# Optimization experiments

Measured on AMD Instinct MI355X. Metric: run time of the kernel, lower is better.

## Reference

```python
import jax, jax.numpy as jnp
import numpy as np

B, S, D_MODEL, H = 2, 2048, 1024, 16
HD = D_MODEL // H  # 64


def rotate_half(x):
    # pairs (x_even, x_odd) -> (-x_odd, x_even), interleaved back
    x1 = x[..., ::2]
    x2 = x[..., 1::2]
    return jnp.stack([-x2, x1], axis=-1).reshape(x.shape)


def rope_sin_cos(seq_len, head_dim):
    pos = jnp.arange(seq_len, dtype=jnp.float32)
    dim = jnp.arange(head_dim, dtype=jnp.float32)
    theta = 10000.0 ** (-2.0 * jnp.floor(dim / 2.0) / head_dim)
    angles = pos[:, None] * theta[None, :]  # [S, HD]
    return jnp.sin(angles), jnp.cos(angles)


def setup_inputs():
    key = jax.random.key(0)
    ks = jax.random.split(key, 6)
    w_scale = 1.0 / np.sqrt(D_MODEL)
    x = jax.random.normal(ks[0], (B, S, D_MODEL), jnp.float32)
    # causal mask: 1.0 where attention is disallowed (j > i)
    mask = (1.0 - jnp.tril(jnp.ones((S, S), jnp.float32)))[None, None, :, :]
    wq = jax.random.normal(ks[1], (D_MODEL, D_MODEL), jnp.float32) * w_scale
    wk = jax.random.normal(ks[2], (D_MODEL, D_MODEL), jnp.float32) * w_scale
    wv = jax.random.normal(ks[3], (D_MODEL, D_MODEL), jnp.float32) * w_scale
    wo = jax.random.normal(ks[4], (D_MODEL, D_MODEL), jnp.float32) * w_scale
    zeros = jnp.zeros((D_MODEL,), jnp.float32)
    return dict(x=x, mask=mask, wq=wq, bq=zeros, wk=wk, bk=zeros,
                wv=wv, bv=zeros, wo=wo, bo=zeros)


def reference(x, mask, wq, bq, wk, bk, wv, bv, wo, bo):
    b, s, _ = x.shape

    def split_heads(t):  # [B,S,D] -> [B,H,S,HD]
        return t.reshape(b, s, H, HD).transpose(0, 2, 1, 3)

    q = split_heads(x @ wq + bq)
    k = split_heads(x @ wk + bk)
    v = split_heads(x @ wv + bv)

    sin, cos = rope_sin_cos(s, HD)
    sin = sin[None, None, :, :]
    cos = cos[None, None, :, :]
    q = q * cos + rotate_half(q) * sin
    k = k * cos + rotate_half(k) * sin

    logits = jnp.einsum('bhqd,bhkd->bhqk', q, k) / jnp.sqrt(jnp.float32(HD))
    logits = logits + mask * (-1e9)
    attn = jax.nn.softmax(logits, axis=-1)
    out = jnp.einsum('bhqk,bhkd->bhqd', attn, v)  # [B,H,S,HD]
    out = out.transpose(0, 2, 1, 3).reshape(b, s, D_MODEL)
    return out @ wo + bo
```

## Files before the change

kernel.cpp:

```cpp
#include <hip/hip_runtime.h>
#include <hip/hip_bf16.h>


#define S_ 2048
#define DM 1024
#define HD 64

typedef __attribute__((ext_vector_type(8))) short short8;
typedef __attribute__((ext_vector_type(4))) short short4v;
typedef __attribute__((ext_vector_type(4))) float floatx4;

__device__ __forceinline__ unsigned short f2b(float x) {
  union { __hip_bfloat16 h; unsigned short u; } cv;
  cv.h = __float2bfloat16(x);
  return cv.u;
}

__device__ __forceinline__ void gload_lds16(const unsigned short* g, unsigned short* l) {
  typedef const __attribute__((address_space(1))) unsigned int* gp_t;
  typedef __attribute__((address_space(3))) unsigned int* lp_t;
  __builtin_amdgcn_global_load_lds((gp_t)(const void*)g, (lp_t)(void*)l, 16, 0, 0);
}

__global__ void cast_kernel(const float* __restrict__ in,
                            unsigned short* __restrict__ out, int n) {
  int i = (blockIdx.x * blockDim.x + threadIdx.x) * 4;
  if (i >= n) return;
  float4 v = *(const float4*)(in + i);
  ushort4 o;
  o.x = f2b(v.x); o.y = f2b(v.y); o.z = f2b(v.z); o.w = f2b(v.w);
  *(ushort4*)(out + i) = o;
}

__global__ void trans_kernel(const float* __restrict__ w0, const float* __restrict__ w1,
                             const float* __restrict__ w2, const float* __restrict__ w3,
                             unsigned short* __restrict__ wt) {
  __shared__ float tile[32][33];
  const float* W = (blockIdx.z == 0) ? w0 : (blockIdx.z == 1) ? w1
                   : (blockIdx.z == 2) ? w2 : w3;
  unsigned short* Wt = wt + (size_t)blockIdx.z * DM * DM;
  const int tx = threadIdx.x & 31;
  const int ty = threadIdx.x >> 5;
  const int k0 = blockIdx.x * 32;
  const int c0 = blockIdx.y * 32;
#pragma unroll
  for (int i = 0; i < 4; ++i)
    tile[ty + i * 8][tx] = W[(size_t)(k0 + ty + i * 8) * DM + c0 + tx];
  __syncthreads();
#pragma unroll
  for (int i = 0; i < 4; ++i)
    Wt[(size_t)(c0 + ty + i * 8) * DM + k0 + tx] = f2b(tile[tx][ty + i * 8]);
}

__global__ void rope_kernel(float2* __restrict__ tab) {
  int i = blockIdx.x * 256 + threadIdx.x;
  int s = i >> 5, d2 = i & 31;
  float th = expf(-(float)d2 * (9.210340371976184f / 32.0f));
  float sn, cs;
  sincosf((float)s * th, &sn, &cs);
  tab[i] = make_float2(cs, sn);
}

__global__ __launch_bounds__(256, 3) void gemm_qkv(
    const unsigned short* __restrict__ A, const unsigned short* __restrict__ Wt,
    const float* __restrict__ bq, const float* __restrict__ bk,
    const float* __restrict__ bv, const float2* __restrict__ rope,
    unsigned short* __restrict__ QKV) {
  __shared__ __attribute__((aligned(16))) unsigned short As[128 * 64];
  __shared__ __attribute__((aligned(16))) unsigned short Bs[128 * 64];
  const int r0 = blockIdx.x * 128;
  const int c0 = blockIdx.y * 128;
  const int t = threadIdx.x;
  const int lane = t & 63;
  const int wv = t >> 6;
  const int wr = (wv >> 1) * 64;
  const int wc = (wv & 1) * 64;
  const int lr = lane & 15;
  const int lg = lane >> 4;

  const int srow = wv * 32 + (lane >> 3);
  const int sseg = ((lane & 7) ^ (lane >> 3)) * 8;
  const unsigned short* Ag = A + (size_t)(r0 + srow) * DM + sseg;
  const unsigned short* Bg = Wt + (size_t)(c0 + srow) * DM + sseg;
  unsigned short* lA = &As[wv * 32 * 64];
  unsigned short* lB = &Bs[wv * 32 * 64];

  floatx4 acc[4][4] = {};
  const int fswz = (lr & 7) << 4;

  for (int k0 = 0; k0 < DM; k0 += 64) {
#pragma unroll
    for (int j = 0; j < 4; ++j) {
      gload_lds16(Ag + k0 + j * 8 * DM, lA + j * 8 * 64);
      gload_lds16(Bg + k0 + j * 8 * DM, lB + j * 8 * 64);
    }
    __syncthreads();
#pragma unroll
    for (int kk = 0; kk < 2; ++kk) {
      short8 af[4], bf[4];
#pragma unroll
      for (int m = 0; m < 4; ++m)
        af[m] = *(const short8*)((char*)As + (wr + m * 16 + lr) * 128 +
                                 ((kk * 64 + lg * 16) ^ fswz));
#pragma unroll
      for (int n = 0; n < 4; ++n)
        bf[n] = *(const short8*)((char*)Bs + (wc + n * 16 + lr) * 128 +
                                 ((kk * 64 + lg * 16) ^ fswz));
#pragma unroll
      for (int m = 0; m < 4; ++m)
#pragma unroll
        for (int n = 0; n < 4; ++n)
          acc[m][n] = __builtin_amdgcn_mfma_f32_16x16x32_bf16(af[m], bf[n], acc[m][n], 0, 0, 0);
    }
    __syncthreads();
  }

  const int mat = blockIdx.y >> 3;
  const float* bias = (mat == 0) ? bq : (mat == 1) ? bk : bv;
  const int rbase = r0 + wr + lg * 4;
  const int cbase = c0 + wc + lr;
#pragma unroll
  for (int n = 0; n < 4; ++n) {
    const int c = cbase + n * 16;
    const int cc = c & (DM - 1);
    const float bvv = bias[cc];
    const int d = c & 63;
    const int h = cc >> 6;
#pragma unroll
    for (int m = 0; m < 4; ++m) {
#pragma unroll
      for (int i = 0; i < 4; ++i) {
        const int r = rbase + m * 16 + i;
        const int s = r & (S_ - 1);
        const int b = r >> 11;
        float v = acc[m][n][i] + bvv;
        float pv = __shfl_xor(v, 1);
        if (mat < 2) {
          float2 cssn = rope[s * 32 + (d >> 1)];
          v = (d & 1) ? fmaf(v, cssn.x, pv * cssn.y) : fmaf(v, cssn.x, -pv * cssn.y);
          if (mat == 0) v *= 0.18033688011112042f;
        }
        QKV[((size_t)((mat << 5) | (b << 4) | h) * S_ + s) * HD + d] = f2b(v);
      }
    }
  }
}

__global__ __launch_bounds__(256, 3) void gemm_out(
    const unsigned short* __restrict__ A, const unsigned short* __restrict__ Wt,
    const float* __restrict__ bias, float* __restrict__ out) {
  __shared__ __attribute__((aligned(16))) unsigned short As[128 * 64];
  __shared__ __attribute__((aligned(16))) unsigned short Bs[128 * 64];
  const int r0 = blockIdx.x * 128;
  const int c0 = blockIdx.y * 128;
  const int t = threadIdx.x;
  const int lane = t & 63;
  const int wv = t >> 6;
  const int wr = (wv >> 1) * 64;
  const int wc = (wv & 1) * 64;
  const int lr = lane & 15;
  const int lg = lane >> 4;

  const int srow = wv * 32 + (lane >> 3);
  const int sseg = ((lane & 7) ^ (lane >> 3)) * 8;
  const unsigned short* Ag = A + (size_t)(r0 + srow) * DM + sseg;
  const unsigned short* Bg = Wt + (size_t)(c0 + srow) * DM + sseg;
  unsigned short* lA = &As[wv * 32 * 64];
  unsigned short* lB = &Bs[wv * 32 * 64];

  floatx4 acc[4][4] = {};
  const int fswz = (lr & 7) << 4;

  for (int k0 = 0; k0 < DM; k0 += 64) {
#pragma unroll
    for (int j = 0; j < 4; ++j) {
      gload_lds16(Ag + k0 + j * 8 * DM, lA + j * 8 * 64);
      gload_lds16(Bg + k0 + j * 8 * DM, lB + j * 8 * 64);
    }
    __syncthreads();
#pragma unroll
    for (int kk = 0; kk < 2; ++kk) {
      short8 af[4], bf[4];
#pragma unroll
      for (int m = 0; m < 4; ++m)
        af[m] = *(const short8*)((char*)As + (wr + m * 16 + lr) * 128 +
                                 ((kk * 64 + lg * 16) ^ fswz));
#pragma unroll
      for (int n = 0; n < 4; ++n)
        bf[n] = *(const short8*)((char*)Bs + (wc + n * 16 + lr) * 128 +
                                 ((kk * 64 + lg * 16) ^ fswz));
#pragma unroll
      for (int m = 0; m < 4; ++m)
#pragma unroll
        for (int n = 0; n < 4; ++n)
          acc[m][n] = __builtin_amdgcn_mfma_f32_16x16x32_bf16(af[m], bf[n], acc[m][n], 0, 0, 0);
    }
    __syncthreads();
  }

  const int rbase = r0 + wr + lg * 4;
  const int cbase = c0 + wc + lr;
#pragma unroll
  for (int n = 0; n < 4; ++n) {
    const int c = cbase + n * 16;
    const float bvv = bias[c];
#pragma unroll
    for (int m = 0; m < 4; ++m) {
#pragma unroll
      for (int i = 0; i < 4; ++i) {
        const int r = rbase + m * 16 + i;
        out[(size_t)r * DM + c] = acc[m][n][i] + bvv;
      }
    }
  }
}

__global__ __launch_bounds__(512, 4) void attn_kernel(
    const unsigned short* __restrict__ Q, const unsigned short* __restrict__ K,
    const unsigned short* __restrict__ V, unsigned short* __restrict__ AttnC) {
  __shared__ __attribute__((aligned(16))) unsigned short Ks[2][64 * 64];
  __shared__ __attribute__((aligned(16))) unsigned short Vs[2][64 * 64];
  __shared__ __attribute__((aligned(16))) unsigned short Ps[8][16 * 64];

  const int bh = blockIdx.x;
  const int qt = 15 - (int)blockIdx.y;
  const int tid = threadIdx.x;
  const int w = tid >> 6;
  const int l = tid & 63;
  const int lg = l >> 4;
  const int lr = l & 15;
  const size_t base = (size_t)bh * S_ * HD;
  const int NT = 2 * qt + 2;
  const int dt = 2 * qt + (w >> 2);
  const int qin = ((w & 3) << 4) + lr;

  short8 qf[2];
  {
    const unsigned short* Qrow =
        Q + base + (size_t)(qt * 128 + w * 16 + lr) * HD + lg * 8;
    qf[0] = *(const short8*)(Qrow);
    qf[1] = *(const short8*)(Qrow + 32);
  }

  floatx4 o[4] = {};
  float m = -1e30f, lsum = 0.f;

  const int krow = tid >> 3;
  const int kseg = tid & 7;
  const int kp = tid & 31;
  const int vd0 = ((tid >> 5) & 7) * 8 + (tid >> 8) * 4;

  int4 kr;
  short4v va, vb;
  {
    const unsigned short* Kg = K + base;
    const unsigned short* Vg = V + base;
    kr = *(const int4*)(Kg + krow * 64 + kseg * 8);
    va = *(const short4v*)(Vg + 2 * kp * 64 + vd0);
    vb = *(const short4v*)(Vg + (2 * kp + 1) * 64 + vd0);
  }

  char* const Pw = (char*)Ps[w];
  const int pswz = (lr & 7) << 4;

  for (int t = 0; t < NT; ++t) {
    const int cur = t & 1;
    {
      char* Kb = (char*)Ks[cur];
      *(int4*)(Kb + krow * 128 + ((kseg * 16) ^ ((krow & 7) << 4))) = kr;
      char* Vb = (char*)Vs[cur];
#pragma unroll
      for (int jj = 0; jj < 4; ++jj) {
        int d = vd0 + jj;
        unsigned int pk = (unsigned int)(unsigned short)va[jj] |
                          ((unsigned int)(unsigned short)vb[jj] << 16);
        *(unsigned int*)(Vb + d * 128 + ((4 * kp) ^ ((d & 7) << 4))) = pk;
      }
    }
    if (t + 1 < NT) {
      const unsigned short* Kg = K + base + (size_t)(t + 1) * 64 * HD;
      const unsigned short* Vg = V + base + (size_t)(t + 1) * 64 * HD;
      kr = *(const int4*)(Kg + krow * 64 + kseg * 8);
      va = *(const short4v*)(Vg + 2 * kp * 64 + vd0);
      vb = *(const short4v*)(Vg + (2 * kp + 1) * 64 + vd0);
    }
    __syncthreads();
    if (t > dt) continue;

    floatx4 s[4] = {};
    __builtin_amdgcn_s_setprio(1);
#pragma unroll
    for (int kk = 0; kk < 2; ++kk) {
#pragma unroll
      for (int n = 0; n < 4; ++n) {
        int r = n * 16 + lr;
        short8 kf = *(const short8*)((char*)Ks[cur] + r * 128 +
                                     ((kk * 64 + lg * 16) ^ ((r & 7) << 4)));
        s[n] = __builtin_amdgcn_mfma_f32_16x16x32_bf16(kf, qf[kk], s[n], 0, 0, 0);
      }
    }
    __builtin_amdgcn_s_setprio(0);
    if (t == dt) {
#pragma unroll
      for (int n = 0; n < 4; ++n)
#pragma unroll
        for (int i = 0; i < 4; ++i)
          if (n * 16 + lg * 4 + i > qin) s[n][i] = -1e30f;
    }

    float tm0 = fmaxf(fmaxf(s[0][0], s[0][1]), fmaxf(s[0][2], s[0][3]));
    float tm1 = fmaxf(fmaxf(s[1][0], s[1][1]), fmaxf(s[1][2], s[1][3]));
    float tm2 = fmaxf(fmaxf(s[2][0], s[2][1]), fmaxf(s[2][2], s[2][3]));
    float tm3 = fmaxf(fmaxf(s[3][0], s[3][1]), fmaxf(s[3][2], s[3][3]));
    float tm = fmaxf(fmaxf(tm0, tm1), fmaxf(tm2, tm3));
    tm = fmaxf(tm, __shfl_xor(tm, 16));
    tm = fmaxf(tm, __shfl_xor(tm, 32));
    if (__any(tm > m + 8.f)) {
      const float mn = fmaxf(m, tm);
      const float al = exp2f(m - mn);
      m = mn;
      lsum *= al;
#pragma unroll
      for (int dd = 0; dd < 4; ++dd) o[dd] *= al;
    }
    float ps = 0.f;
#pragma unroll
    for (int n = 0; n < 4; ++n) {
#pragma unroll
      for (int i = 0; i < 4; ++i) {
        float p = exp2f(s[n][i] - m);
        s[n][i] = p;
        ps += p;
      }
    }
    lsum += ps;

#pragma unroll
    for (int n = 0; n < 4; ++n) {
#pragma unroll
      for (int h = 0; h < 2; ++h) {
        unsigned int pk = (unsigned int)f2b(s[n][2 * h]) |
                          ((unsigned int)f2b(s[n][2 * h + 1]) << 16);
        *(unsigned int*)(Pw + lr * 128 + (((n * 16 + lg * 4 + 2 * h) * 2) ^ pswz)) = pk;
      }
    }
    short8 pb[2];
#pragma unroll
    for (int kk = 0; kk < 2; ++kk)
      pb[kk] = *(const short8*)(Pw + lr * 128 + ((kk * 64 + lg * 16) ^ pswz));
    __builtin_amdgcn_s_setprio(1);
#pragma unroll
    for (int kk = 0; kk < 2; ++kk)
#pragma unroll
      for (int dd = 0; dd < 4; ++dd) {
        int d = dd * 16 + lr;
        short8 vbf = *(const short8*)((char*)Vs[cur] + d * 128 +
                                      ((kk * 64 + lg * 16) ^ ((d & 7) << 4)));
        o[dd] = __builtin_amdgcn_mfma_f32_16x16x32_bf16(vbf, pb[kk], o[dd], 0, 0, 0);
      }
    __builtin_amdgcn_s_setprio(0);
  }

  lsum += __shfl_xor(lsum, 16);
  lsum += __shfl_xor(lsum, 32);
  const float inv = 1.f / lsum;
  unsigned short* orow =
      AttnC + (size_t)((bh >> 4) * S_ + qt * 128 + w * 16 + lr) * DM + (bh & 15) * HD;
#pragma unroll
  for (int dd = 0; dd < 4; ++dd) {
    unsigned int w0 = (unsigned int)f2b(o[dd][0] * inv) |
                      ((unsigned int)f2b(o[dd][1] * inv) << 16);
    unsigned int w1 = (unsigned int)f2b(o[dd][2] * inv) |
                      ((unsigned int)f2b(o[dd][3] * inv) << 16);
    *(uint2*)(orow + dd * 16 + lg * 4) = make_uint2(w0, w1);
  }
}

extern "C" void kernel_launch(void* const* d_in, const int* in_sizes, int n_in,
                              void* d_out, int out_size, void* d_ws, size_t ws_size,
                              hipStream_t stream) {
  const float* x = (const float*)d_in[0];
  const float* wq = (const float*)d_in[2];
  const float* bq = (const float*)d_in[3];
  const float* wk = (const float*)d_in[4];
  const float* bk = (const float*)d_in[5];
  const float* wv = (const float*)d_in[6];
  const float* bv = (const float*)d_in[7];
  const float* wo = (const float*)d_in[8];
  const float* bo = (const float*)d_in[9];

  char* ws = (char*)d_ws;
  const size_t MB = 1024ull * 1024ull;
  unsigned short* Xc = (unsigned short*)(ws);
  unsigned short* Wt = (unsigned short*)(ws + 8 * MB);
  unsigned short* QKVb = (unsigned short*)(ws + 16 * MB);
  unsigned short* Ac = (unsigned short*)(ws + 40 * MB);
  float2* rope = (float2*)(ws + 48 * MB);

  cast_kernel<<<4096, 256, 0, stream>>>(x, Xc, 2 * S_ * DM);
  trans_kernel<<<dim3(32, 32, 4), 256, 0, stream>>>(wq, wk, wv, wo, Wt);
  rope_kernel<<<256, 256, 0, stream>>>(rope);
  gemm_qkv<<<dim3(32, 24), 256, 0, stream>>>(Xc, Wt, bq, bk, bv, rope, QKVb);
  attn_kernel<<<dim3(32, 16), 512, 0, stream>>>(
      QKVb, QKVb + 32ull * S_ * HD, QKVb + 64ull * S_ * HD, Ac);
  gemm_out<<<dim3(32, 8), 256, 0, stream>>>(Ac, Wt + 3ull * DM * DM, bo, (float*)d_out);
}
```

Baseline: 120.5 us.

## Merge prep kernels into one launch and load K fragments directly from global

The cast, weight-transpose and RoPE-table kernels are combined into one prep kernel that dispatches on block index, removing two kernel launches and their gaps. Separately, the attention kernel stops staging K tiles through LDS. Each wave now loads its K MFMA fragments straight from global memory (L2) right before use, which frees LDS space and drops the LDS stores and swizzled reads. In exchange, K loads are no longer prefetched a tile ahead, and the eight waves of a block each read the same K tile redundantly, which may expose global-load latency in the inner loop.

```diff
diff --git a/kernel.cpp b/kernel.cpp
--- a/kernel.cpp
+++ b/kernel.cpp
@@ -22,43 +22,46 @@
   __builtin_amdgcn_global_load_lds((gp_t)(const void*)g, (lp_t)(void*)l, 16, 0, 0);
 }
 
-__global__ void cast_kernel(const float* __restrict__ in,
-                            unsigned short* __restrict__ out, int n) {
-  int i = (blockIdx.x * blockDim.x + threadIdx.x) * 4;
-  if (i >= n) return;
-  float4 v = *(const float4*)(in + i);
-  ushort4 o;
-  o.x = f2b(v.x); o.y = f2b(v.y); o.z = f2b(v.z); o.w = f2b(v.w);
-  *(ushort4*)(out + i) = o;
-}
-
-__global__ void trans_kernel(const float* __restrict__ w0, const float* __restrict__ w1,
-                             const float* __restrict__ w2, const float* __restrict__ w3,
-                             unsigned short* __restrict__ wt) {
-  __shared__ float tile[32][33];
-  const float* W = (blockIdx.z == 0) ? w0 : (blockIdx.z == 1) ? w1
-                   : (blockIdx.z == 2) ? w2 : w3;
-  unsigned short* Wt = wt + (size_t)blockIdx.z * DM * DM;
-  const int tx = threadIdx.x & 31;
-  const int ty = threadIdx.x >> 5;
-  const int k0 = blockIdx.x * 32;
-  const int c0 = blockIdx.y * 32;
-#pragma unroll
-  for (int i = 0; i < 4; ++i)
-    tile[ty + i * 8][tx] = W[(size_t)(k0 + ty + i * 8) * DM + c0 + tx];
-  __syncthreads();
-#pragma unroll
-  for (int i = 0; i < 4; ++i)
-    Wt[(size_t)(c0 + ty + i * 8) * DM + k0 + tx] = f2b(tile[tx][ty + i * 8]);
-}
-
-__global__ void rope_kernel(float2* __restrict__ tab) {
-  int i = blockIdx.x * 256 + threadIdx.x;
-  int s = i >> 5, d2 = i & 31;
-  float th = expf(-(float)d2 * (9.210340371976184f / 32.0f));
-  float sn, cs;
-  sincosf((float)s * th, &sn, &cs);
-  tab[i] = make_float2(cs, sn);
+__global__ void prep_kernel(const float* __restrict__ x,
+                            const float* __restrict__ w0, const float* __restrict__ w1,
+                            const float* __restrict__ w2, const float* __restrict__ w3,
+                            unsigned short* __restrict__ xc,
+                            unsigned short* __restrict__ wt,
+                            float2* __restrict__ rope) {
+  const int bid = blockIdx.x;
+  if (bid < 4096) {
+    int i = (bid * 256 + threadIdx.x) * 4;
+    float4 v = *(const float4*)(x + i);
+    ushort4 o;
+    o.x = f2b(v.x); o.y = f2b(v.y); o.z = f2b(v.z); o.w = f2b(v.w);
+    *(ushort4*)(xc + i) = o;
+  } else if (bid < 8192) {
+    __shared__ float tile[32][33];
+    const int rem = bid - 4096;
+    const int z = rem >> 10;
+    const int bx = (rem & 1023) & 31;
+    const int by = (rem & 1023) >> 5;
+    const float* W = (z == 0) ? w0 : (z == 1) ? w1 : (z == 2) ? w2 : w3;
+    unsigned short* Wt = wt + (size_t)z * DM * DM;
+    const int tx = threadIdx.x & 31;
+    const int ty = threadIdx.x >> 5;
+    const int k0 = bx * 32;
+    const int c0 = by * 32;
+#pragma unroll
+    for (int i = 0; i < 4; ++i)
+      tile[ty + i * 8][tx] = W[(size_t)(k0 + ty + i * 8) * DM + c0 + tx];
+    __syncthreads();
+#pragma unroll
+    for (int i = 0; i < 4; ++i)
+      Wt[(size_t)(c0 + ty + i * 8) * DM + k0 + tx] = f2b(tile[tx][ty + i * 8]);
+  } else {
+    int i = (bid - 8192) * 256 + threadIdx.x;
+    int s = i >> 5, d2 = i & 31;
+    float th = expf(-(float)d2 * (9.210340371976184f / 32.0f));
+    float sn, cs;
+    sincosf((float)s * th, &sn, &cs);
+    rope[i] = make_float2(cs, sn);
+  }
 }
 
 __global__ __launch_bounds__(256, 3) void gemm_qkv(
@@ -218,7 +221,6 @@
 __global__ __launch_bounds__(512, 4) void attn_kernel(
     const unsigned short* __restrict__ Q, const unsigned short* __restrict__ K,
     const unsigned short* __restrict__ V, unsigned short* __restrict__ AttnC) {
-  __shared__ __attribute__((aligned(16))) unsigned short Ks[2][64 * 64];
   __shared__ __attribute__((aligned(16))) unsigned short Vs[2][64 * 64];
   __shared__ __attribute__((aligned(16))) unsigned short Ps[8][16 * 64];
 
@@ -245,17 +247,12 @@
   floatx4 o[4] = {};
   float m = -1e30f, lsum = 0.f;
 
-  const int krow = tid >> 3;
-  const int kseg = tid & 7;
   const int kp = tid & 31;
   const int vd0 = ((tid >> 5) & 7) * 8 + (tid >> 8) * 4;
 
-  int4 kr;
   short4v va, vb;
   {
-    const unsigned short* Kg = K + base;
     const unsigned short* Vg = V + base;
-    kr = *(const int4*)(Kg + krow * 64 + kseg * 8);
     va = *(const short4v*)(Vg + 2 * kp * 64 + vd0);
     vb = *(const short4v*)(Vg + (2 * kp + 1) * 64 + vd0);
   }
@@ -265,9 +262,16 @@
 
   for (int t = 0; t < NT; ++t) {
     const int cur = t & 1;
+    short8 kf[8];
+    if (t <= dt) {
+      const unsigned short* Kt = K + base + (size_t)t * 64 * HD;
+#pragma unroll
+      for (int n = 0; n < 4; ++n)
+#pragma unroll
+        for (int kk = 0; kk < 2; ++kk)
+          kf[n * 2 + kk] = *(const short8*)(Kt + (n * 16 + lr) * HD + kk * 32 + lg * 8);
+    }
     {
-      char* Kb = (char*)Ks[cur];
-      *(int4*)(Kb + krow * 128 + ((kseg * 16) ^ ((krow & 7) << 4))) = kr;
       char* Vb = (char*)Vs[cur];
 #pragma unroll
       for (int jj = 0; jj < 4; ++jj) {
@@ -278,9 +282,7 @@
       }
     }
     if (t + 1 < NT) {
-      const unsigned short* Kg = K + base + (size_t)(t + 1) * 64 * HD;
       const unsigned short* Vg = V + base + (size_t)(t + 1) * 64 * HD;
-      kr = *(const int4*)(Kg + krow * 64 + kseg * 8);
       va = *(const short4v*)(Vg + 2 * kp * 64 + vd0);
       vb = *(const short4v*)(Vg + (2 * kp + 1) * 64 + vd0);
     }
@@ -290,15 +292,10 @@
     floatx4 s[4] = {};
     __builtin_amdgcn_s_setprio(1);
 #pragma unroll
-    for (int kk = 0; kk < 2; ++kk) {
-#pragma unroll
-      for (int n = 0; n < 4; ++n) {
-        int r = n * 16 + lr;
-        short8 kf = *(const short8*)((char*)Ks[cur] + r * 128 +
-                                     ((kk * 64 + lg * 16) ^ ((r & 7) << 4)));
-        s[n] = __builtin_amdgcn_mfma_f32_16x16x32_bf16(kf, qf[kk], s[n], 0, 0, 0);
-      }
-    }
+    for (int kk = 0; kk < 2; ++kk)
+#pragma unroll
+      for (int n = 0; n < 4; ++n)
+        s[n] = __builtin_amdgcn_mfma_f32_16x16x32_bf16(kf[n * 2 + kk], qf[kk], s[n], 0, 0, 0);
     __builtin_amdgcn_s_setprio(0);
     if (t == dt) {
 #pragma unroll
@@ -397,9 +394,7 @@
   unsigned short* Ac = (unsigned short*)(ws + 40 * MB);
   float2* rope = (float2*)(ws + 48 * MB);
 
-  cast_kernel<<<4096, 256, 0, stream>>>(x, Xc, 2 * S_ * DM);
-  trans_kernel<<<dim3(32, 32, 4), 256, 0, stream>>>(wq, wk, wv, wo, Wt);
-  rope_kernel<<<256, 256, 0, stream>>>(rope);
+  prep_kernel<<<8448, 256, 0, stream>>>(x, wq, wk, wv, wo, Xc, Wt, rope);
   gemm_qkv<<<dim3(32, 24), 256, 0, stream>>>(Xc, Wt, bq, bk, bv, rope, QKVb);
   attn_kernel<<<dim3(32, 16), 512, 0, stream>>>(
       QKVb, QKVb + 32ull * S_ * HD, QKVb + 64ull * S_ * HD, Ac);
```

After: 183.8 us. 1.53x slower.
